# Performance work log

Measured on AMD Instinct MI355X. Metric: run time of the kernel, lower is better.

## Reference

```python
import jax, jax.numpy as jnp
import numpy as np

B, N, H = 2, 512, 256


def setup_inputs() -> dict:
    key = jax.random.key(0)
    ks = jax.random.split(key, 12)
    s = 1.0 / np.sqrt(H)
    s2 = 1.0 / np.sqrt(2 * H)
    return {
        "step_sequence": jax.random.normal(ks[0], (B, N, H), dtype=jnp.float32),
        "step_mask": jnp.ones((B, N), dtype=jnp.float32),
        # graph_conv: two Linear(H,H) layers (each followed by ReLU)
        "W_gc1": jax.random.uniform(ks[1], (H, H), minval=-s, maxval=s),
        "b_gc1": jax.random.uniform(ks[2], (H,), minval=-s, maxval=s),
        "W_gc2": jax.random.uniform(ks[3], (H, H), minval=-s, maxval=s),
        "b_gc2": jax.random.uniform(ks[4], (H,), minval=-s, maxval=s),
        # edge_predictor: Linear(2H,H) -> ReLU -> Linear(H,1) -> Sigmoid
        "W_ep1": jax.random.uniform(ks[5], (H, 2 * H), minval=-s2, maxval=s2),
        "b_ep1": jax.random.uniform(ks[6], (H,), minval=-s2, maxval=s2),
        "w_ep2": jax.random.uniform(ks[7], (H,), minval=-s, maxval=s),
        "b_ep2": jax.random.uniform(ks[8], (), minval=-s, maxval=s),
    }


def reference(step_sequence, step_mask, W_gc1, b_gc1, W_gc2, b_gc2,
              W_ep1, b_ep1, w_ep2, b_ep2):
    # graph_conv: (Linear+ReLU) -> ReLU (idempotent) -> (Linear+ReLU)
    h = jax.nn.relu(step_sequence @ W_gc1.T + b_gc1)          # [B,N,H]
    f = jax.nn.relu(h @ W_gc2.T + b_gc2)                       # [B,N,H]
    # edge_predictor on concat(f_i, f_j): split first linear into halves
    Wa, Wb = W_ep1[:, :H], W_ep1[:, H:]
    a = jnp.einsum('bnh,kh->bnk', f, Wa)                       # [B,N,H]
    c = jnp.einsum('bnh,kh->bnk', f, Wb)                       # [B,N,H]
    e = jax.nn.relu(a[:, :, None, :] + c[:, None, :, :] + b_ep1)  # [B,N,N,H]
    scores = jax.nn.sigmoid(jnp.einsum('bijh,h->bij', e, w_ep2) + b_ep2)
    # strictly-lower-triangular causal mask (also zeros the diagonal / i==j)
    mask = jnp.tril(jnp.ones((N, N), dtype=scores.dtype), k=-1)
    return scores * mask
```

## Files before the change

### kernel.cpp

```cpp
#include <hip/hip_runtime.h>
#include <math.h>

#define NSEQ 512
#define MROWS 1024

typedef __attribute__((ext_vector_type(8))) short short8;
typedef __attribute__((ext_vector_type(4))) short short4v;
typedef __attribute__((ext_vector_type(4))) float f32x4;
typedef __attribute__((ext_vector_type(8))) _Float16 half8v;

static __device__ __forceinline__ short f2bf(float f) {
    unsigned u = __float_as_uint(f);
    unsigned r = (u + 0x7fffu + ((u >> 16) & 1u)) >> 16;
    return (short)r;
}
static __device__ __forceinline__ short h2s(_Float16 h) {
    short s; __builtin_memcpy(&s, &h, 2); return s;
}
static __device__ __forceinline__ short8 pack8(float4 a, float4 b) {
    short8 r;
    r[0] = f2bf(a.x); r[1] = f2bf(a.y); r[2] = f2bf(a.z); r[3] = f2bf(a.w);
    r[4] = f2bf(b.x); r[5] = f2bf(b.y); r[6] = f2bf(b.z); r[7] = f2bf(b.w);
    return r;
}
static __device__ __forceinline__ const float* wrow(
    const float* __restrict__ W, int n, int ldw, int colOff) {
    return W + (size_t)(n & 255) * ldw + (size_t)(n >> 8) * colOff;
}

template<int NOUT>
__device__ __forceinline__ void w_load(float4* ra, float4* rb,
    const float* __restrict__ W, int ldw, int colOff, int s, int t)
{
    #pragma unroll
    for (int p = 0; p < NOUT / 128; ++p) {
        const int n = p * 128 + (t >> 2), c = t & 3;
        const float* src = wrow(W, n, ldw, colOff) + s * 32 + c * 8;
        ra[p] = *(const float4*)src;
        rb[p] = *(const float4*)(src + 4);
    }
}
template<int NOUT>
__device__ __forceinline__ void w_store(short* __restrict__ wb,
    const float4* ra, const float4* rb, int t)
{
    #pragma unroll
    for (int p = 0; p < NOUT / 128; ++p) {
        const int n = p * 128 + (t >> 2), c = t & 3;
        *(short8*)&wb[n * 32 + ((c ^ (n & 3)) * 8)] = pack8(ra[p], rb[p]);
    }
}

template<int NOUT, int MODE>
__device__ __forceinline__ void phase(short* wb0, short* wb1,
    const short* __restrict__ actIn, short* __restrict__ actOut,
    const float* __restrict__ W, int ldw, int colOff,
    const float* __restrict__ bias,
    short* __restrict__ Ab, short* __restrict__ Cb, int r0, int t)
{
    constexpr int NT = NOUT / 128;
    {
        float4 ra[NT], rb[NT];
        w_load<NOUT>(ra, rb, W, ldw, colOff, 0, t);
        w_store<NOUT>(wb0, ra, rb, t);
    }
    float4 ra[NT], rb[NT];
    w_load<NOUT>(ra, rb, W, ldw, colOff, 1, t);
    __syncthreads();

    const int w = t >> 6, l = t & 63;
    const int fr = l & 15, fq = l >> 4;
    f32x4 acc[NT];
    #pragma unroll
    for (int i = 0; i < NT; ++i) acc[i] = (f32x4){0.f, 0.f, 0.f, 0.f};

    #pragma unroll
    for (int s = 0; s < 8; ++s) {
        short* cur = (s & 1) ? wb1 : wb0;
        short* nxt = (s & 1) ? wb0 : wb1;
        if (s < 7) {
            w_store<NOUT>(nxt, ra, rb, t);
            if (s < 6) w_load<NOUT>(ra, rb, W, ldw, colOff, s + 2, t);
        }
        const short8 af = *(const short8*)
            &actIn[fr * 256 + ((s * 32 + fq * 8) ^ ((fr & 7) << 3))];
        #pragma unroll
        for (int nt = 0; nt < NT; ++nt) {
            const int n = w * (NT * 16) + nt * 16 + fr;
            const short8 bf = *(const short8*)&cur[n * 32 + ((fq ^ (n & 3)) * 8)];
            acc[nt] = __builtin_amdgcn_mfma_f32_16x16x32_bf16(af, bf, acc[nt], 0, 0, 0);
        }
        __syncthreads();
    }

    #pragma unroll
    for (int nt = 0; nt < NT; ++nt) {
        const int col = w * (NT * 16) + nt * 16 + fr;
        if constexpr (MODE == 0) {
            const float bv = bias[col];
            #pragma unroll
            for (int q = 0; q < 4; ++q) {
                const int row = fq * 4 + q;
                actOut[row * 256 + (col ^ ((row & 7) << 3))] =
                    f2bf(fmaxf(acc[nt][q] + bv, 0.f));
            }
        } else {
            const float bv = (col < 256) ? bias[col] : 0.f;
            #pragma unroll
            for (int q = 0; q < 4; ++q) {
                const int grow = r0 + fq * 4 + q;
                const float v = acc[nt][q] + bv;
                if (col < 256) Ab[(size_t)grow * 256 + col]         = h2s((_Float16)v);
                else           Cb[(size_t)grow * 256 + (col - 256)] = h2s((_Float16)v);
            }
        }
    }
}

__global__ __launch_bounds__(512, 2) void chain_k(
    const float* __restrict__ X,
    const float* __restrict__ W1, const float* __restrict__ b1,
    const float* __restrict__ W2, const float* __restrict__ b2,
    const float* __restrict__ Wep, const float* __restrict__ bep,
    short* __restrict__ Ab, short* __restrict__ Cb)
{
    __shared__ short wb[2][16384];
    __shared__ short act[2][4096];

    const int t  = threadIdx.x;
    const int r0 = (int)blockIdx.x * 16;

    {
        const int row = t >> 5, c = t & 31;
        const float* src = X + (size_t)(r0 + row) * 256 + c * 8;
        float4 v0 = *(const float4*)src, v1 = *(const float4*)(src + 4);
        *(short8*)&act[0][row * 256 + ((c ^ (row & 7)) * 8)] = pack8(v0, v1);
    }
    phase<256, 0>(wb[0], wb[1], act[0], act[1], W1, 256, 0, b1,
                  nullptr, nullptr, r0, t);
    phase<256, 0>(wb[0], wb[1], act[1], act[0], W2, 256, 0, b2,
                  nullptr, nullptr, r0, t);
    phase<512, 1>(wb[0], wb[1], act[0], nullptr, Wep, 512, 256, bep,
                  Ab, Cb, r0, t);
}

__device__ __forceinline__ float dot8(half8v x, half8v w, float s) {
    s = __builtin_amdgcn_fdot2(__builtin_shufflevector(x, x, 0, 1),
                               __builtin_shufflevector(w, w, 0, 1), s, false);
    s = __builtin_amdgcn_fdot2(__builtin_shufflevector(x, x, 2, 3),
                               __builtin_shufflevector(w, w, 2, 3), s, false);
    s = __builtin_amdgcn_fdot2(__builtin_shufflevector(x, x, 4, 5),
                               __builtin_shufflevector(w, w, 4, 5), s, false);
    s = __builtin_amdgcn_fdot2(__builtin_shufflevector(x, x, 6, 7),
                               __builtin_shufflevector(w, w, 6, 7), s, false);
    return s;
}

__global__ __launch_bounds__(256) void pair_k(
    const short* __restrict__ Ab, const short* __restrict__ Cb,
    const float* __restrict__ wv, const float* __restrict__ b2p,
    float* __restrict__ out)
{
    __shared__ short lds[4][2 * 16 * 256 + 256];

    const int t    = threadIdx.x;
    const int wave = t >> 6, l = t & 63;
    const int tile = (int)blockIdx.x * 4 + wave;
    const int b    = tile >> 10;
    const int r_   = tile & 1023;
    const int it   = r_ >> 5, jt = r_ & 31;
    const int i0   = it * 16, j0 = jt * 16;
    float* outb = out + (size_t)b * NSEQ * NSEQ;

    if (jt > it) {
        const int rr = l >> 2, cc = (l & 3) * 4;
        *(float4*)(outb + (size_t)(i0 + rr) * NSEQ + j0 + cc) =
            make_float4(0.f, 0.f, 0.f, 0.f);
        return;
    }

    short* A_l = &lds[wave][0];
    short* C_l = &lds[wave][16 * 256];
    short* W_l = &lds[wave][2 * 16 * 256];

    {
        const int lrow = l >> 5;
        const int cc   = l & 31;
        const size_t abase = (size_t)(b * NSEQ + i0) * 256;
        const size_t cbase = (size_t)(b * NSEQ + j0) * 256;
        short8 areg[8], creg[8];
        #pragma unroll
        for (int q = 0; q < 8; ++q) {
            const int row = q * 2 + lrow;
            areg[q] = *(const short8*)(Ab + abase + row * 256 + cc * 8);
            creg[q] = *(const short8*)(Cb + cbase + row * 256 + cc * 8);
        }
        float4 w4 = *(const float4*)(wv + l * 4);
        #pragma unroll
        for (int q = 0; q < 8; ++q) {
            const int row = q * 2 + lrow;
            const int sw  = (cc ^ (row & 7)) * 8;
            *(short8*)&A_l[row * 256 + sw] = areg[q];
            *(short8*)&C_l[row * 256 + sw] = creg[q];
        }
        short4v wp;
        wp.x = h2s((_Float16)w4.x); wp.y = h2s((_Float16)w4.y);
        wp.z = h2s((_Float16)w4.z); wp.w = h2s((_Float16)w4.w);
        *(short4v*)&W_l[l * 4] = wp;
    }

    const int ti = l >> 3, tj = l & 7;
    float s00 = 0.f, s01 = 0.f, s10 = 0.f, s11 = 0.f;
    const half8v z8 = (half8v)(_Float16)0.f;

    #pragma unroll 8
    for (int cc = 0; cc < 32; ++cc) {
        half8v a0 = *(const half8v*)&A_l[ ti      * 256 + ((cc ^ ( ti      & 7)) * 8)];
        half8v a1 = *(const half8v*)&A_l[(ti + 8) * 256 + ((cc ^ ((ti + 8) & 7)) * 8)];
        half8v c0 = *(const half8v*)&C_l[ tj      * 256 + ((cc ^ ( tj      & 7)) * 8)];
        half8v c1 = *(const half8v*)&C_l[(tj + 8) * 256 + ((cc ^ ((tj + 8) & 7)) * 8)];
        half8v w8 = *(const half8v*)&W_l[cc * 8];
        half8v x;
        x = __builtin_elementwise_max(a0 + c0, z8); s00 = dot8(x, w8, s00);
        x = __builtin_elementwise_max(a0 + c1, z8); s01 = dot8(x, w8, s01);
        x = __builtin_elementwise_max(a1 + c0, z8); s10 = dot8(x, w8, s10);
        x = __builtin_elementwise_max(a1 + c1, z8); s11 = dot8(x, w8, s11);
    }

    const float bias2 = *b2p;
    const int i1 = i0 + ti, i2 = i0 + ti + 8;
    const int j1 = j0 + tj, j2 = j0 + tj + 8;
    const float r00 = 1.f / (1.f + expf(-(s00 + bias2)));
    const float r01 = 1.f / (1.f + expf(-(s01 + bias2)));
    const float r10 = 1.f / (1.f + expf(-(s10 + bias2)));
    const float r11 = 1.f / (1.f + expf(-(s11 + bias2)));
    outb[(size_t)i1 * NSEQ + j1] = (j1 < i1) ? r00 : 0.f;
    outb[(size_t)i1 * NSEQ + j2] = (j2 < i1) ? r01 : 0.f;
    outb[(size_t)i2 * NSEQ + j1] = (j1 < i2) ? r10 : 0.f;
    outb[(size_t)i2 * NSEQ + j2] = (j2 < i2) ? r11 : 0.f;
}

extern "C" void kernel_launch(void* const* d_in, const int* in_sizes, int n_in,
                              void* d_out, int out_size, void* d_ws, size_t ws_size,
                              hipStream_t stream)
{
    (void)in_sizes; (void)n_in; (void)out_size; (void)ws_size;
    const float* X    = (const float*)d_in[0];
    const float* Wg1  = (const float*)d_in[2];
    const float* bg1  = (const float*)d_in[3];
    const float* Wg2  = (const float*)d_in[4];
    const float* bg2  = (const float*)d_in[5];
    const float* Wep1 = (const float*)d_in[6];
    const float* bep1 = (const float*)d_in[7];
    const float* wep2 = (const float*)d_in[8];
    const float* bep2 = (const float*)d_in[9];
    float* out = (float*)d_out;

    short* Ab = (short*)d_ws;
    short* Cb = Ab + MROWS * 256;

    hipLaunchKernelGGL(chain_k, dim3(64), dim3(512), 0, stream,
                       X, Wg1, bg1, Wg2, bg2, Wep1, bep1, Ab, Cb);
    hipLaunchKernelGGL(pair_k, dim3(512), dim3(256), 0, stream,
                       Ab, Cb, wep2, bep2, out);
}
```

Measured before the change: 29.25 us.

## Double chain kernel block to 1024 threads and widen weight k-slices

The fused MLP chain kernel now runs with 1024 threads per block, so each wave owns fewer output tiles. The weight staging is parameterized by a k-slice width BK: 64 for the two graph-conv layers (4 stages instead of 8) and 32 for the edge-predictor projection. Fewer stages mean fewer barriers and more loads in flight per step, which targets the latency-bound chain on only 64 blocks. In exchange it raises register and barrier pressure, since 1024 threads now synchronize, and it drops the occupancy hint of two blocks per CU.

```diff
diff --git a/kernel.cpp b/kernel.cpp
--- a/kernel.cpp
+++ b/kernel.cpp
@@ -28,44 +28,41 @@
     return W + (size_t)(n & 255) * ldw + (size_t)(n >> 8) * colOff;
 }
 
-template<int NOUT>
-__device__ __forceinline__ void w_load(float4* ra, float4* rb,
-    const float* __restrict__ W, int ldw, int colOff, int s, int t)
-{
-    #pragma unroll
-    for (int p = 0; p < NOUT / 128; ++p) {
-        const int n = p * 128 + (t >> 2), c = t & 3;
-        const float* src = wrow(W, n, ldw, colOff) + s * 32 + c * 8;
-        ra[p] = *(const float4*)src;
-        rb[p] = *(const float4*)(src + 4);
-    }
-}
-template<int NOUT>
-__device__ __forceinline__ void w_store(short* __restrict__ wb,
-    const float4* ra, const float4* rb, int t)
-{
-    #pragma unroll
-    for (int p = 0; p < NOUT / 128; ++p) {
-        const int n = p * 128 + (t >> 2), c = t & 3;
-        *(short8*)&wb[n * 32 + ((c ^ (n & 3)) * 8)] = pack8(ra[p], rb[p]);
-    }
-}
-
-template<int NOUT, int MODE>
-__device__ __forceinline__ void phase(short* wb0, short* wb1,
+template<int NOUT, int BK, int MODE>
+__device__ __forceinline__ void phase(
+    short* __restrict__ wb0, short* __restrict__ wb1,
     const short* __restrict__ actIn, short* __restrict__ actOut,
     const float* __restrict__ W, int ldw, int colOff,
     const float* __restrict__ bias,
     short* __restrict__ Ab, short* __restrict__ Cb, int r0, int t)
 {
-    constexpr int NT = NOUT / 128;
-    {
-        float4 ra[NT], rb[NT];
-        w_load<NOUT>(ra, rb, W, ldw, colOff, 0, t);
-        w_store<NOUT>(wb0, ra, rb, t);
-    }
-    float4 ra[NT], rb[NT];
-    w_load<NOUT>(ra, rb, W, ldw, colOff, 1, t);
+    constexpr int CH = BK / 8;
+    constexpr int KM = CH - 1;
+    constexpr int NS = 256 / BK;
+    constexpr int NT = NOUT / 256;
+
+    float4 r[4];
+    auto wload = [&](int s) {
+        #pragma unroll
+        for (int j = 0; j < 2; ++j) {
+            const int id = t * 2 + j;
+            const int n = id / CH, kc = id % CH;
+            const float* src = wrow(W, n, ldw, colOff) + s * BK + kc * 8;
+            r[j * 2]     = *(const float4*)src;
+            r[j * 2 + 1] = *(const float4*)(src + 4);
+        }
+    };
+    auto wstore = [&](short* __restrict__ wb) {
+        #pragma unroll
+        for (int j = 0; j < 2; ++j) {
+            const int id = t * 2 + j;
+            const int n = id / CH, kc = id % CH;
+            *(short8*)&wb[n * BK + ((kc ^ (n & KM)) * 8)] = pack8(r[j * 2], r[j * 2 + 1]);
+        }
+    };
+
+    wload(0); wstore(wb0);
+    if (NS > 1) wload(1);
     __syncthreads();
 
     const int w = t >> 6, l = t & 63;
@@ -75,20 +72,25 @@
     for (int i = 0; i < NT; ++i) acc[i] = (f32x4){0.f, 0.f, 0.f, 0.f};
 
     #pragma unroll
-    for (int s = 0; s < 8; ++s) {
+    for (int s = 0; s < NS; ++s) {
         short* cur = (s & 1) ? wb1 : wb0;
         short* nxt = (s & 1) ? wb0 : wb1;
-        if (s < 7) {
-            w_store<NOUT>(nxt, ra, rb, t);
-            if (s < 6) w_load<NOUT>(ra, rb, W, ldw, colOff, s + 2, t);
-        }
-        const short8 af = *(const short8*)
-            &actIn[fr * 256 + ((s * 32 + fq * 8) ^ ((fr & 7) << 3))];
-        #pragma unroll
-        for (int nt = 0; nt < NT; ++nt) {
-            const int n = w * (NT * 16) + nt * 16 + fr;
-            const short8 bf = *(const short8*)&cur[n * 32 + ((fq ^ (n & 3)) * 8)];
-            acc[nt] = __builtin_amdgcn_mfma_f32_16x16x32_bf16(af, bf, acc[nt], 0, 0, 0);
+        if (s < NS - 1) {
+            wstore(nxt);
+            if (s < NS - 2) wload(s + 2);
+        }
+        #pragma unroll
+        for (int h = 0; h < BK / 32; ++h) {
+            const int gchunk = s * CH + h * 4 + fq;
+            const short8 af = *(const short8*)
+                &actIn[fr * 256 + ((gchunk ^ (fr & 7)) * 8)];
+            #pragma unroll
+            for (int nt = 0; nt < NT; ++nt) {
+                const int n = w * (NT * 16) + nt * 16 + fr;
+                const short8 bf = *(const short8*)
+                    &cur[n * BK + (((h * 4 + fq) ^ (n & KM)) * 8)];
+                acc[nt] = __builtin_amdgcn_mfma_f32_16x16x32_bf16(af, bf, acc[nt], 0, 0, 0);
+            }
         }
         __syncthreads();
     }
@@ -117,7 +119,7 @@
     }
 }
 
-__global__ __launch_bounds__(512, 2) void chain_k(
+__global__ __launch_bounds__(1024) void chain_k(
     const float* __restrict__ X,
     const float* __restrict__ W1, const float* __restrict__ b1,
     const float* __restrict__ W2, const float* __restrict__ b2,
@@ -130,18 +132,18 @@
     const int t  = threadIdx.x;
     const int r0 = (int)blockIdx.x * 16;
 
-    {
+    if (t < 512) {
         const int row = t >> 5, c = t & 31;
         const float* src = X + (size_t)(r0 + row) * 256 + c * 8;
         float4 v0 = *(const float4*)src, v1 = *(const float4*)(src + 4);
         *(short8*)&act[0][row * 256 + ((c ^ (row & 7)) * 8)] = pack8(v0, v1);
     }
-    phase<256, 0>(wb[0], wb[1], act[0], act[1], W1, 256, 0, b1,
-                  nullptr, nullptr, r0, t);
-    phase<256, 0>(wb[0], wb[1], act[1], act[0], W2, 256, 0, b2,
-                  nullptr, nullptr, r0, t);
-    phase<512, 1>(wb[0], wb[1], act[0], nullptr, Wep, 512, 256, bep,
-                  Ab, Cb, r0, t);
+    phase<256, 64, 0>(wb[0], wb[1], act[0], act[1], W1, 256, 0, b1,
+                      nullptr, nullptr, r0, t);
+    phase<256, 64, 0>(wb[0], wb[1], act[1], act[0], W2, 256, 0, b2,
+                      nullptr, nullptr, r0, t);
+    phase<512, 32, 1>(wb[0], wb[1], act[0], nullptr, Wep, 512, 256, bep,
+                      Ab, Cb, r0, t);
 }
 
 __device__ __forceinline__ float dot8(half8v x, half8v w, float s) {
@@ -259,7 +261,7 @@
     short* Ab = (short*)d_ws;
     short* Cb = Ab + MROWS * 256;
 
-    hipLaunchKernelGGL(chain_k, dim3(64), dim3(512), 0, stream,
+    hipLaunchKernelGGL(chain_k, dim3(64), dim3(1024), 0, stream,
                        X, Wg1, bg1, Wg2, bg2, Wep1, bep1, Ab, Cb);
     hipLaunchKernelGGL(pair_k, dim3(512), dim3(256), 0, stream,
                        Ab, Cb, wep2, bep2, out);
```

New measurement: 33.84 us. 15.7% more time.
